# Kernel tuning notes

Measured on AMD Instinct MI355X. Metric: run time of the kernel, lower is better.

Reference implementation:

```python
import jax, jax.numpy as jnp
import numpy as np

NUM_CLASSES = 1000
FEAT_DIM = 256
MOMENTUM = 0.999
WARMUP_STEPS = 200


def setup_inputs() -> dict:
    key = jax.random.key(0)
    k1, k2, k3, k4, k5 = jax.random.split(key, 5)
    N, B, K = 200000, 64, 100
    features = jax.random.normal(k1, (N, FEAT_DIM), jnp.float32)
    labels = jax.random.randint(k2, (N,), 0, NUM_CLASSES)
    labels_per_image = jax.random.randint(k3, (B, K), 0, NUM_CLASSES)
    prototypes = jax.random.normal(k4, (NUM_CLASSES, FEAT_DIM), jnp.float32)
    init_mask = jax.random.randint(k5, (NUM_CLASSES,), 0, 2).astype(jnp.int32)
    cooccurrence = jnp.zeros((NUM_CLASSES, NUM_CLASSES), jnp.float32)
    return dict(features=features, labels=labels, labels_per_image=labels_per_image,
                prototypes=prototypes, init_mask=init_mask, cooccurrence=cooccurrence,
                step=5000)


def reference(features, labels, labels_per_image, prototypes, init_mask, cooccurrence, step):
    C = prototypes.shape[0]
    progress = min(1.0, float(step) / max(1, WARMUP_STEPS * 10))
    m = 0.99 + (MOMENTUM - 0.99) * progress

    # F.normalize(features, dim=-1) with eps=1e-12
    fn = features / jnp.clip(jnp.linalg.norm(features, axis=-1, keepdims=True), 1e-12)

    # per-class scatter-mean (replaces Python loop over labels.unique())
    counts = jax.ops.segment_sum(jnp.ones(labels.shape, jnp.float32), labels, num_segments=C)  # [C]
    sums = jax.ops.segment_sum(fn, labels, num_segments=C)                                      # [C, D]
    mean = sums / jnp.maximum(counts, 1.0)[:, None]

    present = (counts > 0)[:, None]          # class appears in this batch
    inited = (init_mask > 0)[:, None]        # prototype already initialized
    ema = m * prototypes + (1.0 - m) * mean
    new_protos = jnp.where(present & inited, ema, jnp.where(present & ~inited, mean, prototypes))
    new_init = ((init_mask > 0) | (counts > 0)).astype(jnp.int32)

    # co-occurrence: presence matrix P[B,C]; pair (ci,cj) gets +1 each direction per image
    B, K = labels_per_image.shape
    rows = jnp.repeat(jnp.arange(B), K)
    P = jnp.zeros((B, C), jnp.float32).at[rows, labels_per_image.reshape(-1)].set(1.0)
    cooc_add = (P.T @ P) * (1.0 - jnp.eye(C, dtype=jnp.float32))
    new_cooc = cooccurrence + cooc_add

    return new_protos, new_init, new_cooc
```

## Files before the change

### kernel.cpp

```cpp
#include <hip/hip_runtime.h>
#include <hip/hip_bf16.h>

#define NC 1000
#define FD 256
#define KPI 100

__global__ void k_hist(const int* __restrict__ labels, int n,
                       const int* __restrict__ lpi, int bk,
                       int* __restrict__ counts,
                       unsigned long long* __restrict__ M) {
    int i = blockIdx.x * blockDim.x + threadIdx.x;
    if (i < n) atomicAdd(&counts[labels[i]], 1);
    if (i < bk) {
        int b = i / KPI;
        atomicOr(&M[lpi[i]], 1ull << b);
    }
}

__global__ void k_scan(const int* __restrict__ counts, int* __restrict__ offsets) {
    __shared__ int sh[1024];
    int tid = threadIdx.x;
    int v = (tid < NC) ? counts[tid] : 0;
    sh[tid] = v;
    __syncthreads();
    for (int off = 1; off < 1024; off <<= 1) {
        int t = (tid >= off) ? sh[tid - off] : 0;
        __syncthreads();
        sh[tid] += t;
        __syncthreads();
    }
    if (tid < NC) offsets[tid] = sh[tid] - v;
}

__global__ void k_scatter(const int* __restrict__ labels, int n,
                          const int* __restrict__ offsets,
                          int* __restrict__ cursor, int* __restrict__ rowidx) {
    int i = blockIdx.x * blockDim.x + threadIdx.x;
    if (i < n) {
        int lab = labels[i];
        int pos = offsets[lab] + atomicAdd(&cursor[lab], 1);
        rowidx[pos] = i;
    }
}

__global__ __launch_bounds__(256) void k_proto(
    const float* __restrict__ feat, const int* __restrict__ rowidx,
    const int* __restrict__ offsets, const int* __restrict__ counts,
    const float* __restrict__ protos, const int* __restrict__ init_mask,
    const int* __restrict__ step,
    float* __restrict__ out_protos, float* __restrict__ out_init) {
    int c = blockIdx.x;
    int tid = threadIdx.x;
    int lane = tid & 63;
    int w = tid >> 6;
    int start = offsets[c];
    int cnt = counts[c];
    int end = start + cnt;

    const float4* f4 = (const float4*)feat;
    float ax = 0.f, ay = 0.f, az = 0.f, aw = 0.f;

    for (int base = start + 2 * w; base < end; base += 8) {
        int r0 = rowidx[base];
        bool ok1 = (base + 1) < end;
        int r1 = ok1 ? rowidx[base + 1] : r0;
        float4 a = f4[(size_t)r0 * 64 + lane];
        float4 b = f4[(size_t)r1 * 64 + lane];
        float s0 = a.x * a.x + a.y * a.y + a.z * a.z + a.w * a.w;
        float s1 = b.x * b.x + b.y * b.y + b.z * b.z + b.w * b.w;
        #pragma unroll
        for (int o = 32; o; o >>= 1) {
            s0 += __shfl_xor(s0, o);
            s1 += __shfl_xor(s1, o);
        }
        float sc0 = 1.0f / fmaxf(sqrtf(s0), 1e-12f);
        float sc1 = ok1 ? (1.0f / fmaxf(sqrtf(s1), 1e-12f)) : 0.0f;
        ax += a.x * sc0 + b.x * sc1;
        ay += a.y * sc0 + b.y * sc1;
        az += a.z * sc0 + b.z * sc1;
        aw += a.w * sc0 + b.w * sc1;
    }

    __shared__ float sh[1024];
    int e = lane * 4;
    sh[w * 256 + e + 0] = ax;
    sh[w * 256 + e + 1] = ay;
    sh[w * 256 + e + 2] = az;
    sh[w * 256 + e + 3] = aw;
    __syncthreads();

    int d = tid;
    float t = sh[d] + sh[256 + d] + sh[512 + d] + sh[768 + d];
    float mean = t / fmaxf((float)cnt, 1.0f);

    float p = protos[c * FD + d];
    bool present = cnt > 0;
    bool inited = init_mask[c] > 0;
    float prog = fminf(1.0f, (float)step[0] / 2000.0f);
    float m = 0.99f + (0.999f - 0.99f) * prog;
    float ema = m * p + (1.0f - m) * mean;
    float outv = present ? (inited ? ema : mean) : p;
    out_protos[c * FD + d] = outv;
    if (tid == 0) out_init[c] = (inited || present) ? 1.0f : 0.0f;
}

__global__ void k_cooc(const unsigned long long* __restrict__ M,
                       const float* __restrict__ cooc_in,
                       float* __restrict__ cooc_out) {
    int j = blockIdx.x * blockDim.x + threadIdx.x;
    int i = blockIdx.y;
    if (j < NC) {
        unsigned long long mi = M[i];
        unsigned long long mj = M[j];
        float add = (i == j) ? 0.0f : (float)__popcll(mi & mj);
        cooc_out[i * NC + j] = cooc_in[i * NC + j] + add;
    }
}

extern "C" void kernel_launch(void* const* d_in, const int* in_sizes, int n_in,
                              void* d_out, int out_size, void* d_ws, size_t ws_size,
                              hipStream_t stream) {
    const float* feat      = (const float*)d_in[0];
    const int*   labels    = (const int*)d_in[1];
    const int*   lpi       = (const int*)d_in[2];
    const float* protos    = (const float*)d_in[3];
    const int*   init_mask = (const int*)d_in[4];
    const float* cooc      = (const float*)d_in[5];
    const int*   step      = (const int*)d_in[6];

    int n  = in_sizes[1];
    int bk = in_sizes[2];

    float* out_protos = (float*)d_out;
    float* out_init   = out_protos + (size_t)NC * FD;
    float* out_cooc   = out_init + NC;

    char* ws = (char*)d_ws;
    int* counts                = (int*)(ws);
    int* cursor                = (int*)(ws + 4096);
    unsigned long long* M      = (unsigned long long*)(ws + 8192);
    int* offsets               = (int*)(ws + 16384);
    int* rowidx                = (int*)(ws + 20480);

    hipMemsetAsync(d_ws, 0, 16384, stream);

    int big = n > bk ? n : bk;
    k_hist<<<(big + 255) / 256, 256, 0, stream>>>(labels, n, lpi, bk, counts, M);
    k_scan<<<1, 1024, 0, stream>>>(counts, offsets);
    k_scatter<<<(n + 255) / 256, 256, 0, stream>>>(labels, n, offsets, cursor, rowidx);
    k_proto<<<NC, 256, 0, stream>>>(feat, rowidx, offsets, counts, protos, init_mask,
                                    step, out_protos, out_init);
    k_cooc<<<dim3((NC + 255) / 256, NC), 256, 0, stream>>>(M, cooc, out_cooc);
}
```

Baseline: 399.8 us.

## Fuse scan with co-occurrence kernel, seed cursors with offsets, unroll proto gather 4x

```diff
diff --git a/kernel.cpp b/kernel.cpp
--- a/kernel.cpp
+++ b/kernel.cpp
@@ -11,34 +11,45 @@
                        unsigned long long* __restrict__ M) {
     int i = blockIdx.x * blockDim.x + threadIdx.x;
     if (i < n) atomicAdd(&counts[labels[i]], 1);
-    if (i < bk) {
-        int b = i / KPI;
-        atomicOr(&M[lpi[i]], 1ull << b);
+    if (i < bk) atomicOr(&M[lpi[i]], 1ull << (i / KPI));
+}
+
+__global__ __launch_bounds__(1024) void k_scan_cooc(
+    const int* __restrict__ counts,
+    int* __restrict__ offsets, int* __restrict__ cursor,
+    const unsigned long long* __restrict__ M,
+    const float* __restrict__ cooc_in, float* __restrict__ cooc_out) {
+    int tid = threadIdx.x;
+    if (blockIdx.x == NC) {
+        __shared__ int sh[1024];
+        int v = (tid < NC) ? counts[tid] : 0;
+        sh[tid] = v;
+        __syncthreads();
+        for (int off = 1; off < 1024; off <<= 1) {
+            int t = (tid >= off) ? sh[tid - off] : 0;
+            __syncthreads();
+            sh[tid] += t;
+            __syncthreads();
+        }
+        if (tid < NC) {
+            int e = sh[tid] - v;
+            offsets[tid] = e;
+            cursor[tid] = e;
+        }
+    } else {
+        int i = blockIdx.x;
+        if (tid < NC) {
+            float add = (i == tid) ? 0.0f : (float)__popcll(M[i] & M[tid]);
+            cooc_out[i * NC + tid] = cooc_in[i * NC + tid] + add;
+        }
     }
 }
 
-__global__ void k_scan(const int* __restrict__ counts, int* __restrict__ offsets) {
-    __shared__ int sh[1024];
-    int tid = threadIdx.x;
-    int v = (tid < NC) ? counts[tid] : 0;
-    sh[tid] = v;
-    __syncthreads();
-    for (int off = 1; off < 1024; off <<= 1) {
-        int t = (tid >= off) ? sh[tid - off] : 0;
-        __syncthreads();
-        sh[tid] += t;
-        __syncthreads();
-    }
-    if (tid < NC) offsets[tid] = sh[tid] - v;
-}
-
 __global__ void k_scatter(const int* __restrict__ labels, int n,
-                          const int* __restrict__ offsets,
                           int* __restrict__ cursor, int* __restrict__ rowidx) {
     int i = blockIdx.x * blockDim.x + threadIdx.x;
     if (i < n) {
-        int lab = labels[i];
-        int pos = offsets[lab] + atomicAdd(&cursor[lab], 1);
+        int pos = atomicAdd(&cursor[labels[i]], 1);
         rowidx[pos] = i;
     }
 }
@@ -60,37 +71,42 @@
     const float4* f4 = (const float4*)feat;
     float ax = 0.f, ay = 0.f, az = 0.f, aw = 0.f;
 
-    for (int base = start + 2 * w; base < end; base += 8) {
-        int r0 = rowidx[base];
-        bool ok1 = (base + 1) < end;
-        int r1 = ok1 ? rowidx[base + 1] : r0;
-        float4 a = f4[(size_t)r0 * 64 + lane];
-        float4 b = f4[(size_t)r1 * 64 + lane];
-        float s0 = a.x * a.x + a.y * a.y + a.z * a.z + a.w * a.w;
-        float s1 = b.x * b.x + b.y * b.y + b.z * b.z + b.w * b.w;
+    for (int base = start + 4 * w; base < end; base += 16) {
+        int r[4];
+        float4 v[4];
+        float s[4];
+        #pragma unroll
+        for (int k = 0; k < 4; k++) {
+            int idx = (base + k < end) ? (base + k) : (end - 1);
+            r[k] = rowidx[idx];
+        }
+        #pragma unroll
+        for (int k = 0; k < 4; k++) v[k] = f4[(size_t)r[k] * 64 + lane];
+        #pragma unroll
+        for (int k = 0; k < 4; k++)
+            s[k] = v[k].x * v[k].x + v[k].y * v[k].y + v[k].z * v[k].z + v[k].w * v[k].w;
         #pragma unroll
         for (int o = 32; o; o >>= 1) {
-            s0 += __shfl_xor(s0, o);
-            s1 += __shfl_xor(s1, o);
+            #pragma unroll
+            for (int k = 0; k < 4; k++) s[k] += __shfl_xor(s[k], o);
         }
-        float sc0 = 1.0f / fmaxf(sqrtf(s0), 1e-12f);
-        float sc1 = ok1 ? (1.0f / fmaxf(sqrtf(s1), 1e-12f)) : 0.0f;
-        ax += a.x * sc0 + b.x * sc1;
-        ay += a.y * sc0 + b.y * sc1;
-        az += a.z * sc0 + b.z * sc1;
-        aw += a.w * sc0 + b.w * sc1;
+        #pragma unroll
+        for (int k = 0; k < 4; k++) {
+            float sc = (base + k < end) ? (1.0f / fmaxf(sqrtf(s[k]), 1e-12f)) : 0.0f;
+            ax += v[k].x * sc;
+            ay += v[k].y * sc;
+            az += v[k].z * sc;
+            aw += v[k].w * sc;
+        }
     }
 
-    __shared__ float sh[1024];
-    int e = lane * 4;
-    sh[w * 256 + e + 0] = ax;
-    sh[w * 256 + e + 1] = ay;
-    sh[w * 256 + e + 2] = az;
-    sh[w * 256 + e + 3] = aw;
+    __shared__ float4 sh4[256];
+    sh4[w * 64 + lane] = make_float4(ax, ay, az, aw);
     __syncthreads();
 
+    const float* shf = (const float*)sh4;
     int d = tid;
-    float t = sh[d] + sh[256 + d] + sh[512 + d] + sh[768 + d];
+    float t = shf[d] + shf[256 + d] + shf[512 + d] + shf[768 + d];
     float mean = t / fmaxf((float)cnt, 1.0f);
 
     float p = protos[c * FD + d];
@@ -102,19 +118,6 @@
     float outv = present ? (inited ? ema : mean) : p;
     out_protos[c * FD + d] = outv;
     if (tid == 0) out_init[c] = (inited || present) ? 1.0f : 0.0f;
-}
-
-__global__ void k_cooc(const unsigned long long* __restrict__ M,
-                       const float* __restrict__ cooc_in,
-                       float* __restrict__ cooc_out) {
-    int j = blockIdx.x * blockDim.x + threadIdx.x;
-    int i = blockIdx.y;
-    if (j < NC) {
-        unsigned long long mi = M[i];
-        unsigned long long mj = M[j];
-        float add = (i == j) ? 0.0f : (float)__popcll(mi & mj);
-        cooc_out[i * NC + j] = cooc_in[i * NC + j] + add;
-    }
 }
 
 extern "C" void kernel_launch(void* const* d_in, const int* in_sizes, int n_in,
@@ -136,19 +139,18 @@
     float* out_cooc   = out_init + NC;
 
     char* ws = (char*)d_ws;
-    int* counts                = (int*)(ws);
-    int* cursor                = (int*)(ws + 4096);
-    unsigned long long* M      = (unsigned long long*)(ws + 8192);
-    int* offsets               = (int*)(ws + 16384);
-    int* rowidx                = (int*)(ws + 20480);
+    int* counts           = (int*)(ws);
+    int* cursor           = (int*)(ws + 4096);
+    unsigned long long* M = (unsigned long long*)(ws + 8192);
+    int* offsets          = (int*)(ws + 16384);
+    int* rowidx           = (int*)(ws + 20480);
 
     hipMemsetAsync(d_ws, 0, 16384, stream);
 
     int big = n > bk ? n : bk;
     k_hist<<<(big + 255) / 256, 256, 0, stream>>>(labels, n, lpi, bk, counts, M);
-    k_scan<<<1, 1024, 0, stream>>>(counts, offsets);
-    k_scatter<<<(n + 255) / 256, 256, 0, stream>>>(labels, n, offsets, cursor, rowidx);
+    k_scan_cooc<<<NC + 1, 1024, 0, stream>>>(counts, offsets, cursor, M, cooc, out_cooc);
+    k_scatter<<<(n + 255) / 256, 256, 0, stream>>>(labels, n, cursor, rowidx);
     k_proto<<<NC, 256, 0, stream>>>(feat, rowidx, offsets, counts, protos, init_mask,
                                     step, out_protos, out_init);
-    k_cooc<<<dim3((NC + 255) / 256, NC), 256, 0, stream>>>(M, cooc, out_cooc);
 }
```

Result: faster. 388.2 us (-2.9%).
